# Performance work log

Measured on AMD Instinct MI355X. Metric: run time of the kernel, lower is better.

Reference implementation:

```python
import jax, jax.numpy as jnp
import numpy as np

BASE = 10000.0

def rotate_half(x):
    # interleaved pairs: (x0, x1, x2, x3, ...) -> (-x1, x0, -x3, x2, ...)
    x2 = x.reshape(x.shape[:-1] + (-1, 2))
    a, b = x2[..., 0], x2[..., 1]
    return jnp.stack((-b, a), axis=-1).reshape(x.shape)

def rope_tables(seq_len, head_dim, dtype):
    inv_freq = 1.0 / (BASE ** (jnp.arange(0, head_dim, 2, dtype=jnp.float32) / head_dim))
    t = jnp.arange(seq_len, dtype=jnp.float32)
    freqs = jnp.outer(t, inv_freq)                      # [s, head_dim//2]
    cos = jnp.repeat(jnp.cos(freqs), 2, axis=-1)        # '... d -> ... (d 2)'
    sin = jnp.repeat(jnp.sin(freqs), 2, axis=-1)
    # seq_dimension = -3 for [b, s, h, d] tensors -> broadcast over heads
    return cos[:, None, :].astype(dtype), sin[:, None, :].astype(dtype)

def setup_inputs() -> dict:
    key = jax.random.key(0)
    kx, kw1, kw2 = jax.random.split(key, 3)
    b, s, d = 4, 2048, 2048
    h = 16
    x = jax.random.normal(kx, (b, s, d), dtype=jnp.float32)
    # causal mask: True above the diagonal = masked positions
    attn_mask = jnp.triu(jnp.ones((s, s), dtype=bool), k=1)
    Wqkv_w = jax.random.normal(kw1, (d, 3 * d), dtype=jnp.float32) / np.sqrt(d)
    Wqkv_b = jnp.zeros((3 * d,), dtype=jnp.float32)
    Wout_w = jax.random.normal(kw2, (d, d), dtype=jnp.float32) / np.sqrt(d)
    Wout_b = jnp.zeros((d,), dtype=jnp.float32)
    return {"x": x, "attn_mask": attn_mask, "Wqkv_w": Wqkv_w, "Wqkv_b": Wqkv_b,
            "Wout_w": Wout_w, "Wout_b": Wout_b, "num_heads": 16}

def reference(x, attn_mask, Wqkv_w, Wqkv_b, Wout_w, Wout_b, num_heads):
    b, s, d = x.shape
    h = num_heads
    hd = d // h
    qkv = jnp.einsum('bsd,de->bse', x, Wqkv_w) + Wqkv_b        # [b, s, 3d]
    qkv = qkv.reshape(b, s, 3, h, hd)
    q, k, v = qkv[:, :, 0], qkv[:, :, 1], qkv[:, :, 2]          # [b, s, h, hd]
    cos, sin = rope_tables(s, hd, x.dtype)                      # [s, 1, hd]
    q = q * cos + rotate_half(q) * sin
    k = k * cos + rotate_half(k) * sin
    scale = 1.0 / np.sqrt(hd).astype(np.float32)
    scores = jnp.einsum('bqhd,bkhd->bhqk', q, k) * scale        # [b, h, s, s]
    scores = jnp.where(attn_mask, -jnp.inf, scores)
    attn = jax.nn.softmax(scores, axis=-1)
    ctx = jnp.einsum('bhqk,bkhd->bqhd', attn, v)                # [b, s, h, hd]
    ctx = ctx.reshape(b, s, d)
    return jnp.einsum('bsd,de->bse', ctx, Wout_w) + Wout_b
```

## Files before the change

kernel.cpp:

```cpp
#include <hip/hip_runtime.h>

#define BB 4
#define SS 2048
#define DD 2048
#define HH 16
#define HD 128
#define D3 6144

typedef __attribute__((ext_vector_type(8))) short short8;
typedef __attribute__((ext_vector_type(4))) float float4v;

#define MFMA16(a, b, c) __builtin_amdgcn_mfma_f32_16x16x32_bf16(a, b, c, 0, 0, 0)

#define GLL16(g, l)                                                     \
    __builtin_amdgcn_global_load_lds(                                   \
        (__attribute__((address_space(1))) void*)(g),                   \
        (__attribute__((address_space(3))) void*)(l), 16, 0, 0)

__device__ __forceinline__ unsigned short f2b(float f) {
    union { float f; unsigned u; } v;
    v.f = f;
    unsigned r = v.u + 0x7FFFu + ((v.u >> 16) & 1u);
    return (unsigned short)(r >> 16);
}
__device__ __forceinline__ float b2f(unsigned short h) {
    union { unsigned u; float f; } v;
    v.u = ((unsigned)h) << 16;
    return v.f;
}

__global__ void cast_f32_bf16(const float* __restrict__ in,
                              unsigned short* __restrict__ out) {
    int i = (blockIdx.x * 256 + threadIdx.x) * 4;
    float4 v = *(const float4*)(in + i);
    ushort4 o;
    o.x = f2b(v.x); o.y = f2b(v.y); o.z = f2b(v.z); o.w = f2b(v.w);
    *(ushort4*)(out + i) = o;
}

__global__ void transpose_cast(const float* __restrict__ in,
                               unsigned short* __restrict__ out, int R, int C) {
    __shared__ float tile[32][33];
    int c0 = blockIdx.x * 32, r0 = blockIdx.y * 32;
    int tc = threadIdx.x & 31, tr = threadIdx.x >> 5;
#pragma unroll
    for (int i = 0; i < 4; ++i) {
        int r = tr + i * 8;
        tile[r][tc] = in[(size_t)(r0 + r) * C + c0 + tc];
    }
    __syncthreads();
#pragma unroll
    for (int i = 0; i < 4; ++i) {
        int wr = tr + i * 8;
        out[(size_t)(c0 + wr) * R + r0 + tc] = f2b(tile[tc][wr]);
    }
}

__global__ void vtrans(const unsigned short* __restrict__ qkv,
                       unsigned short* __restrict__ vT) {
    __shared__ unsigned short tile[32][33];
    int bh = blockIdx.z, b = bh >> 4, h = bh & 15;
    int s0 = blockIdx.x * 32, d0 = blockIdx.y * 32;
    int tc = threadIdx.x & 31, tr = threadIdx.x >> 5;
    const unsigned short* src = qkv + (size_t)b * SS * D3 + 4096 + h * HD;
#pragma unroll
    for (int i = 0; i < 4; ++i) {
        int sl = tr + i * 8;
        tile[sl][tc] = src[(size_t)(s0 + sl) * D3 + d0 + tc];
    }
    __syncthreads();
    unsigned short* dst = vT + (size_t)bh * HD * SS;
#pragma unroll
    for (int i = 0; i < 4; ++i) {
        int dl = tr + i * 8;
        dst[(size_t)(d0 + dl) * SS + s0 + tc] = tile[tc][dl];
    }
}

template <int BF16OUT>
__global__ __launch_bounds__(256) void gemm_bt(
    const unsigned short* __restrict__ A,
    const unsigned short* __restrict__ Bt,
    const float* __restrict__ bias,
    void* __restrict__ Cout, int M, int N, int K) {
    __shared__ unsigned short As[128 * 32];
    __shared__ unsigned short Bs[128 * 32];
    const int n0 = blockIdx.x * 128, m0 = blockIdx.y * 128;
    const int t = threadIdx.x, lane = t & 63, w = t >> 6;
    const int quad = lane >> 4, lr = lane & 15;
    const int wm = (w >> 1) * 64, wn = (w & 1) * 64;
    float4v acc[4][4] = {};
    const int srow = w * 32 + (lane >> 2);
    const int scol = (lane & 3) * 8;
    const unsigned short* Ag = A + (size_t)(m0 + srow) * K + scol;
    const unsigned short* Bg = Bt + (size_t)(n0 + srow) * K + scol;
    unsigned short* Asw = &As[(w * 32) * 32];
    unsigned short* Bsw = &Bs[(w * 32) * 32];
    for (int k0 = 0; k0 < K; k0 += 32) {
        __syncthreads();
        GLL16(Ag + k0, Asw);
        GLL16(Ag + k0 + (size_t)16 * K, Asw + 16 * 32);
        GLL16(Bg + k0, Bsw);
        GLL16(Bg + k0 + (size_t)16 * K, Bsw + 16 * 32);
        __syncthreads();
        short8 af[4], bf[4];
#pragma unroll
        for (int i = 0; i < 4; ++i)
            af[i] = *(const short8*)&As[(wm + i * 16 + lr) * 32 + quad * 8];
#pragma unroll
        for (int j = 0; j < 4; ++j)
            bf[j] = *(const short8*)&Bs[(wn + j * 16 + lr) * 32 + quad * 8];
#pragma unroll
        for (int i = 0; i < 4; ++i)
#pragma unroll
            for (int j = 0; j < 4; ++j)
                acc[i][j] = MFMA16(af[i], bf[j], acc[i][j]);
    }
#pragma unroll
    for (int j = 0; j < 4; ++j) {
        int n = n0 + wn + j * 16 + lr;
        float bv = bias[n];
#pragma unroll
        for (int i = 0; i < 4; ++i)
#pragma unroll
            for (int r = 0; r < 4; ++r) {
                int m = m0 + wm + i * 16 + quad * 4 + r;
                float v = acc[i][j][r] + bv;
                if (BF16OUT)
                    ((unsigned short*)Cout)[(size_t)m * N + n] = f2b(v);
                else
                    ((float*)Cout)[(size_t)m * N + n] = v;
            }
    }
}

__global__ void rope_kernel(unsigned short* __restrict__ qkv) {
    int tid = blockIdx.x * 256 + threadIdx.x;
    int i4 = tid & 15;
    int h = (tid >> 4) & 15;
    int s = (tid >> 8) & 2047;
    int b = tid >> 19;
    size_t off = ((size_t)(b * SS + s)) * D3 + h * HD + i4 * 8;
    unsigned short* q = qkv + off;
    unsigned short* k = q + 2048;
    short8 qv = *(short8*)q, kv = *(short8*)k;
    const float L2IF = 0.2076205059304601f;
    const float R2PI = 0.15915494309189535f;
    short8 qo, ko;
#pragma unroll
    for (int j = 0; j < 4; ++j) {
        int i = i4 * 4 + j;
        float invr = exp2f(-(float)i * L2IF) * R2PI;
        float rev = (float)s * invr;
        float rr = rev - floorf(rev);
        float sn = __builtin_amdgcn_sinf(rr);
        float cs = __builtin_amdgcn_cosf(rr);
        float a0 = b2f((unsigned short)qv[2 * j]);
        float a1 = b2f((unsigned short)qv[2 * j + 1]);
        qo[2 * j] = (short)f2b(a0 * cs - a1 * sn);
        qo[2 * j + 1] = (short)f2b(a1 * cs + a0 * sn);
        float c0 = b2f((unsigned short)kv[2 * j]);
        float c1 = b2f((unsigned short)kv[2 * j + 1]);
        ko[2 * j] = (short)f2b(c0 * cs - c1 * sn);
        ko[2 * j + 1] = (short)f2b(c1 * cs + c0 * sn);
    }
    *(short8*)q = qo;
    *(short8*)k = ko;
}

__global__ __launch_bounds__(256) void attn_kernel(
    const unsigned short* __restrict__ qkv,
    const unsigned short* __restrict__ vT,
    unsigned short* __restrict__ ctx) {
    __shared__ unsigned short Ks[2][64 * 128];
    __shared__ unsigned short Vs[2][128 * 64];
    __shared__ unsigned short PT[4][32][40];
    const int bh = blockIdx.y, b = bh >> 4, h = bh & 15;
    const int t = threadIdx.x, w = t >> 6, lane = t & 63;
    const int quad = lane >> 4, lr = lane & 15;
    const unsigned short* qbase = qkv + (size_t)b * SS * D3 + h * HD;
    const unsigned short* kbase = qbase + 2048;
    const unsigned short* vtb = vT + (size_t)bh * HD * SS;
    const float SCL2E = 0.12751741769976451f;
    const float NB16 = -23.083120654223414f;
    const int q0a = blockIdx.x * 128;
    const int q0b = (15 - (int)blockIdx.x) * 128;
    const int nta = (q0a >> 6) + 2, ntb = (q0b >> 6) + 2, ntot = nta + ntb;
    const int kr = lane >> 4, kg = lane & 15;
    const int vr = lane >> 3, vg = lane & 7;

    auto stage = [&](int k0, int bi) {
        unsigned short* KD = Ks[bi];
        unsigned short* VD = Vs[bi];
#pragma unroll
        for (int u = 0; u < 4; ++u) {
            int row = w * 16 + u * 4 + kr;
            int g = kg ^ (row & 15);
            GLL16(kbase + (size_t)(k0 + row) * D3 + g * 8,
                  &KD[(w * 16 + u * 4) * 128]);
        }
#pragma unroll
        for (int u = 0; u < 4; ++u) {
            int row = w * 32 + u * 8 + vr;
            int g = vg ^ (row & 7);
            GLL16(vtb + (size_t)row * SS + k0 + g * 8,
                  &VD[(w * 32 + u * 8) * 64]);
        }
    };

    int wq = q0a + w * 32;
    short8 qf[2][4];
#pragma unroll
    for (int m = 0; m < 2; ++m)
#pragma unroll
        for (int c = 0; c < 4; ++c)
            qf[m][c] = *(const short8*)(qbase + (size_t)(wq + m * 16 + lr) * D3 +
                                        c * 32 + quad * 8);

    float4v o[2][8] = {};
    float l_lane[2] = {0.f, 0.f};

    auto epilogue = [&]() {
#pragma unroll
        for (int m = 0; m < 2; ++m) {
            float l = l_lane[m];
            l += __shfl_xor(l, 16);
            l += __shfl_xor(l, 32);
#pragma unroll
            for (int r = 0; r < 4; ++r) {
                float linv = 1.0f / __shfl(l, quad * 4 + r);
#pragma unroll
                for (int dc = 0; dc < 8; ++dc) {
                    float val = o[m][dc][r] * linv;
                    ctx[(size_t)(b * SS + wq + m * 16 + quad * 4 + r) * DD +
                        h * HD + dc * 16 + lr] = f2b(val);
                }
            }
        }
    };

    stage(0, 0);

    for (int it = 0; it < ntot; ++it) {
        __syncthreads();
        int nit = it + 1;
        if (nit < ntot) stage((nit < nta ? nit : nit - nta) * 64, nit & 1);
        int k0 = (it < nta ? it : it - nta) * 64;
        const unsigned short* KB = Ks[it & 1];
        const unsigned short* VB = Vs[it & 1];

        if (k0 <= wq + 31) {
            float4v sc[2][4] = {};
#pragma unroll
            for (int c = 0; c < 4; ++c) {
                short8 kf[4];
#pragma unroll
                for (int ks = 0; ks < 4; ++ks)
                    kf[ks] = *(const short8*)&KB[(ks * 16 + lr) * 128 +
                                                 (((c * 4 + quad) ^ lr) * 8)];
#pragma unroll
                for (int ks = 0; ks < 4; ++ks) {
                    sc[0][ks] = MFMA16(kf[ks], qf[0][c], sc[0][ks]);
                    sc[1][ks] = MFMA16(kf[ks], qf[1][c], sc[1][ks]);
                }
            }
            const bool nm = (k0 + 63 > wq);
#pragma unroll
            for (int kc = 0; kc < 2; ++kc) {
#pragma unroll
                for (int m = 0; m < 2; ++m)
#pragma unroll
                    for (int ks2 = 0; ks2 < 2; ++ks2) {
                        int ks = kc * 2 + ks2;
                        unsigned pk[2];
#pragma unroll
                        for (int rp = 0; rp < 2; ++rp) {
                            unsigned lo = 0, hi = 0;
#pragma unroll
                            for (int rr = 0; rr < 2; ++rr) {
                                int r = rp * 2 + rr;
                                float p = exp2f(fmaf(sc[m][ks][r], SCL2E, NB16));
                                if (nm) {
                                    int key = k0 + ks * 16 + quad * 4 + r;
                                    if (key > wq + m * 16 + lr) p = 0.0f;
                                }
                                l_lane[m] += p;
                                union { float f; unsigned u; } pu;
                                pu.f = p;
                                if (rr == 0) lo = pu.u >> 16;
                                else hi = pu.u >> 16;
                            }
                            pk[rp] = lo | (hi << 16);
                        }
                        uint2 pkk = {pk[0], pk[1]};
                        *(uint2*)&PT[w][m * 16 + lr][ks2 * 16 + quad * 4] = pkk;
                    }
                short8 pf0 = *(const short8*)&PT[w][lr][quad * 8];
                short8 pf1 = *(const short8*)&PT[w][16 + lr][quad * 8];
#pragma unroll
                for (int dc = 0; dc < 8; ++dc) {
                    short8 vf = *(const short8*)&VB[(dc * 16 + lr) * 64 +
                                                    (((kc * 4 + quad) ^ (lr & 7)) * 8)];
                    o[0][dc] = MFMA16(pf0, vf, o[0][dc]);
                    o[1][dc] = MFMA16(pf1, vf, o[1][dc]);
                }
            }
        }

        if (it == nta - 1) {
            epilogue();
#pragma unroll
            for (int m = 0; m < 2; ++m) {
                l_lane[m] = 0.f;
#pragma unroll
                for (int dc = 0; dc < 8; ++dc) o[m][dc] = (float4v){0, 0, 0, 0};
            }
            wq = q0b + w * 32;
#pragma unroll
            for (int m = 0; m < 2; ++m)
#pragma unroll
                for (int c = 0; c < 4; ++c)
                    qf[m][c] = *(const short8*)(qbase +
                                                (size_t)(wq + m * 16 + lr) * D3 +
                                                c * 32 + quad * 8);
        }
    }
    epilogue();
}

extern "C" void kernel_launch(void* const* d_in, const int* in_sizes, int n_in,
                              void* d_out, int out_size, void* d_ws, size_t ws_size,
                              hipStream_t stream) {
    const float* x = (const float*)d_in[0];
    const float* Wqkv_w = (const float*)d_in[2];
    const float* Wqkv_b = (const float*)d_in[3];
    const float* Wout_w = (const float*)d_in[4];
    const float* Wout_b = (const float*)d_in[5];
    float* out = (float*)d_out;

    unsigned short* x_bf = (unsigned short*)d_ws;
    unsigned short* wqkv_t = x_bf + 16777216;
    unsigned short* wout_t = wqkv_t + 12582912;
    unsigned short* qkv = wout_t + 4194304;
    unsigned short* ctx = qkv + 50331648;
    unsigned short* vT = x_bf;

    cast_f32_bf16<<<16384, 256, 0, stream>>>(x, x_bf);
    transpose_cast<<<dim3(192, 64), 256, 0, stream>>>(Wqkv_w, wqkv_t, 2048, 6144);
    transpose_cast<<<dim3(64, 64), 256, 0, stream>>>(Wout_w, wout_t, 2048, 2048);
    gemm_bt<1><<<dim3(48, 64), 256, 0, stream>>>(x_bf, wqkv_t, Wqkv_b, qkv,
                                                 8192, 6144, 2048);
    rope_kernel<<<8192, 256, 0, stream>>>(qkv);
    vtrans<<<dim3(64, 4, 64), 256, 0, stream>>>(qkv, vT);
    attn_kernel<<<dim3(8, 64), 256, 0, stream>>>(qkv, vT, ctx);
    gemm_bt<0><<<dim3(16, 64), 256, 0, stream>>>(ctx, wout_t, Wout_b, out,
                                                 8192, 2048, 2048);
}
```

Baseline: 758.3 us.

## Replace 128x128 GEMM with double-buffered 256x256 tile GEMM using swizzled LDS

Rewrites the projection GEMM to use 256x256 output tiles with 512 threads, BK=64, and LDS double buffering via global_load_lds. It adds an XOR swizzle to avoid LDS bank conflicts, an XCD-aware remapping of workgroup IDs, and interleaves MFMA phases with barriers and setprio. The aim is more data reuse per loaded byte and overlap of global loads with compute, at the cost of 128KB of LDS and heavier register pressure per block.

```diff
diff --git a/kernel.cpp b/kernel.cpp
--- a/kernel.cpp
+++ b/kernel.cpp
@@ -78,60 +78,129 @@
 }
 
 template <int BF16OUT>
-__global__ __launch_bounds__(256) void gemm_bt(
+__global__ __launch_bounds__(512, 2) void gemm256(
     const unsigned short* __restrict__ A,
     const unsigned short* __restrict__ Bt,
     const float* __restrict__ bias,
     void* __restrict__ Cout, int M, int N, int K) {
-    __shared__ unsigned short As[128 * 32];
-    __shared__ unsigned short Bs[128 * 32];
-    const int n0 = blockIdx.x * 128, m0 = blockIdx.y * 128;
+    __shared__ unsigned short As[2][256 * 64];
+    __shared__ unsigned short Bs[2][256 * 64];
+
+    const int nbx = N >> 8;
+    const int lin = blockIdx.y * nbx + blockIdx.x;
+    const int cpx = (nbx * (M >> 8)) >> 3;
+    const int wg = (lin & 7) * cpx + (lin >> 3);
+    const int n0 = (wg % nbx) * 256, m0 = (wg / nbx) * 256;
+
     const int t = threadIdx.x, lane = t & 63, w = t >> 6;
     const int quad = lane >> 4, lr = lane & 15;
-    const int wm = (w >> 1) * 64, wn = (w & 1) * 64;
-    float4v acc[4][4] = {};
-    const int srow = w * 32 + (lane >> 2);
-    const int scol = (lane & 3) * 8;
-    const unsigned short* Ag = A + (size_t)(m0 + srow) * K + scol;
-    const unsigned short* Bg = Bt + (size_t)(n0 + srow) * K + scol;
-    unsigned short* Asw = &As[(w * 32) * 32];
-    unsigned short* Bsw = &Bs[(w * 32) * 32];
-    for (int k0 = 0; k0 < K; k0 += 32) {
-        __syncthreads();
-        GLL16(Ag + k0, Asw);
-        GLL16(Ag + k0 + (size_t)16 * K, Asw + 16 * 32);
-        GLL16(Bg + k0, Bsw);
-        GLL16(Bg + k0 + (size_t)16 * K, Bsw + 16 * 32);
-        __syncthreads();
-        short8 af[4], bf[4];
-#pragma unroll
-        for (int i = 0; i < 4; ++i)
-            af[i] = *(const short8*)&As[(wm + i * 16 + lr) * 32 + quad * 8];
-#pragma unroll
-        for (int j = 0; j < 4; ++j)
-            bf[j] = *(const short8*)&Bs[(wn + j * 16 + lr) * 32 + quad * 8];
-#pragma unroll
-        for (int i = 0; i < 4; ++i)
-#pragma unroll
-            for (int j = 0; j < 4; ++j)
-                acc[i][j] = MFMA16(af[i], bf[j], acc[i][j]);
-    }
-#pragma unroll
-    for (int j = 0; j < 4; ++j) {
-        int n = n0 + wn + j * 16 + lr;
-        float bv = bias[n];
-#pragma unroll
-        for (int i = 0; i < 4; ++i)
+    const int wm = (w >> 2) * 128, wn = (w & 3) * 64;
+
+    const int sr = lane >> 3;
+    const int ss = (lane & 7) ^ sr;
+    const unsigned short* Ag = A + (size_t)(m0 + w * 32 + sr) * K + ss * 8;
+    const unsigned short* Bg = Bt + (size_t)(n0 + w * 32 + sr) * K + ss * 8;
+
+    float4v acc[8][4] = {};
+    short8 af[4][2], b0[2][2], b1[2][2];
+
+#define STAGE_A(buf, k0)                                                     \
+    do {                                                                     \
+        _Pragma("unroll") for (int r = 0; r < 4; ++r)                        \
+            GLL16(Ag + (k0) + (size_t)r * 8 * K,                             \
+                  &As[buf][(w * 32 + r * 8) * 64]);                          \
+    } while (0)
+#define STAGE_B(buf, k0)                                                     \
+    do {                                                                     \
+        _Pragma("unroll") for (int r = 0; r < 4; ++r)                        \
+            GLL16(Bg + (k0) + (size_t)r * 8 * K,                             \
+                  &Bs[buf][(w * 32 + r * 8) * 64]);                          \
+    } while (0)
+#define LDA(dst, mh)                                                         \
+    do {                                                                     \
+        _Pragma("unroll") for (int i = 0; i < 4; ++i)                        \
+            _Pragma("unroll") for (int kk = 0; kk < 2; ++kk)                 \
+                dst[i][kk] = *(const short8*)&As[cur][                       \
+                    (wm + (mh)*64 + i * 16 + lr) * 64 +                      \
+                    (((kk * 4 + quad) ^ (lr & 7)) * 8)];                     \
+    } while (0)
+#define LDB(dst, nh)                                                         \
+    do {                                                                     \
+        _Pragma("unroll") for (int j = 0; j < 2; ++j)                        \
+            _Pragma("unroll") for (int kk = 0; kk < 2; ++kk)                 \
+                dst[j][kk] = *(const short8*)&Bs[cur][                       \
+                    (wn + (nh)*32 + j * 16 + lr) * 64 +                      \
+                    (((kk * 4 + quad) ^ (lr & 7)) * 8)];                     \
+    } while (0)
+#define MM(ar, br, io, jo)                                                   \
+    do {                                                                     \
+        __builtin_amdgcn_s_setprio(1);                                       \
+        _Pragma("unroll") for (int kk = 0; kk < 2; ++kk)                     \
+            _Pragma("unroll") for (int i = 0; i < 4; ++i)                    \
+                _Pragma("unroll") for (int j = 0; j < 2; ++j)                \
+                    acc[(io) + i][(jo) + j] = MFMA16(                        \
+                        ar[i][kk], br[j][kk], acc[(io) + i][(jo) + j]);      \
+        __builtin_amdgcn_s_setprio(0);                                       \
+    } while (0)
+
+    const int NT = K >> 6;
+    STAGE_A(0, 0);
+    STAGE_B(0, 0);
+
+    for (int tk = 0; tk < NT; ++tk) {
+        const int cur = tk & 1, nxt = cur ^ 1;
+        const size_t k0n = (size_t)(tk + 1 == NT ? 0 : tk + 1) << 6;
+
+        STAGE_A(nxt, k0n);
+        asm volatile("s_waitcnt vmcnt(4)" ::: "memory");
+        __builtin_amdgcn_s_barrier();
+        __builtin_amdgcn_sched_barrier(0);
+        LDA(af, 0);
+        LDB(b0, 0);
+        __builtin_amdgcn_s_barrier();
+        asm volatile("s_waitcnt lgkmcnt(0)" ::: "memory");
+        __builtin_amdgcn_sched_barrier(0);
+        MM(af, b0, 0, 0);
+        __builtin_amdgcn_s_barrier();
+        STAGE_B(nxt, k0n);
+        LDB(b1, 1);
+        __builtin_amdgcn_s_barrier();
+        asm volatile("s_waitcnt lgkmcnt(0)" ::: "memory");
+        __builtin_amdgcn_sched_barrier(0);
+        MM(af, b1, 0, 2);
+        __builtin_amdgcn_s_barrier();
+        LDA(af, 1);
+        __builtin_amdgcn_s_barrier();
+        asm volatile("s_waitcnt lgkmcnt(0)" ::: "memory");
+        __builtin_amdgcn_sched_barrier(0);
+        MM(af, b0, 4, 0);
+        __builtin_amdgcn_s_barrier();
+        MM(af, b1, 4, 2);
+        __builtin_amdgcn_s_barrier();
+    }
+    asm volatile("s_waitcnt vmcnt(0)" ::: "memory");
+
+#pragma unroll
+    for (int jj = 0; jj < 4; ++jj) {
+        const int n = n0 + wn + jj * 16 + lr;
+        const float bv = bias[n];
+#pragma unroll
+        for (int ii = 0; ii < 8; ++ii)
 #pragma unroll
             for (int r = 0; r < 4; ++r) {
-                int m = m0 + wm + i * 16 + quad * 4 + r;
-                float v = acc[i][j][r] + bv;
+                const int m = m0 + wm + ii * 16 + quad * 4 + r;
+                const float v = acc[ii][jj][r] + bv;
                 if (BF16OUT)
                     ((unsigned short*)Cout)[(size_t)m * N + n] = f2b(v);
                 else
                     ((float*)Cout)[(size_t)m * N + n] = v;
             }
     }
+#undef STAGE_A
+#undef STAGE_B
+#undef LDA
+#undef LDB
+#undef MM
 }
 
 __global__ void rope_kernel(unsigned short* __restrict__ qkv) {
@@ -348,11 +417,11 @@
     cast_f32_bf16<<<16384, 256, 0, stream>>>(x, x_bf);
     transpose_cast<<<dim3(192, 64), 256, 0, stream>>>(Wqkv_w, wqkv_t, 2048, 6144);
     transpose_cast<<<dim3(64, 64), 256, 0, stream>>>(Wout_w, wout_t, 2048, 2048);
-    gemm_bt<1><<<dim3(48, 64), 256, 0, stream>>>(x_bf, wqkv_t, Wqkv_b, qkv,
+    gemm256<1><<<dim3(24, 32), 512, 0, stream>>>(x_bf, wqkv_t, Wqkv_b, qkv,
                                                  8192, 6144, 2048);
     rope_kernel<<<8192, 256, 0, stream>>>(qkv);
     vtrans<<<dim3(64, 4, 64), 256, 0, stream>>>(qkv, vT);
     attn_kernel<<<dim3(8, 64), 256, 0, stream>>>(qkv, vT, ctx);
-    gemm_bt<0><<<dim3(16, 64), 256, 0, stream>>>(ctx, wout_t, Wout_b, out,
-                                                 8192, 2048, 2048);
-}
+    gemm256<0><<<dim3(8, 32), 512, 0, stream>>>(ctx, wout_t, Wout_b, out,
+                                                8192, 2048, 2048);
+}
```

After: 786.0 us. 1.04x slower.
